# Kernel optimization log

Measured on AMD Instinct MI355X. Metric: run time of the kernel, lower is better.

## Reference

```python
import jax, jax.numpy as jnp
import numpy as np


def _sqdist(X1, X2):
    # squared euclidean distance matrix, matches torch.cdist(...,p=2)**2
    d2 = (jnp.sum(X1 * X1, -1)[:, None] + jnp.sum(X2 * X2, -1)[None, :]
          - 2.0 * (X1 @ X2.T))
    return jnp.maximum(d2, 0.0)


def setup_inputs() -> dict:
    key = jax.random.key(0)
    k1, k2, k3, k4, k5, k6 = jax.random.split(key, 6)
    n, m, d, C = 1024, 2048, 4, 64
    X_train = jax.random.normal(k1, (n, d), dtype=jnp.float32)
    y_train = jax.random.normal(k2, (n,), dtype=jnp.float32)
    X_test = jax.random.normal(k3, (m, d), dtype=jnp.float32)
    # positive params within the priors' supports
    lengthscale = jax.random.uniform(k4, (C,), minval=0.1, maxval=3.0, dtype=jnp.float32)
    variance = jax.random.uniform(k5, (C,), minval=0.1, maxval=3.0, dtype=jnp.float32)
    noise = jax.random.uniform(k6, (C,), minval=0.01, maxval=0.5, dtype=jnp.float32)
    return {"X_train": X_train, "y_train": y_train, "X_test": X_test,
            "lengthscale": lengthscale, "variance": variance, "noise": noise}


def reference(X_train, y_train, X_test, lengthscale, variance, noise):
    n = X_train.shape[0]
    ls2 = (lengthscale ** 2)[:, None, None]          # [C,1,1]
    var = variance[:, None, None]                     # [C,1,1]
    d2_tr = _sqdist(X_train, X_train)                 # [n,n]
    d2_te = _sqdist(X_test, X_train)                  # [m,n]
    K_train = var * jnp.exp(-0.5 * d2_tr[None] / ls2)   # [C,n,n]
    K_test = var * jnp.exp(-0.5 * d2_te[None] / ls2)    # [C,m,n]
    K_noisy = K_train + noise[:, None, None] * jnp.eye(n, dtype=K_train.dtype)
    L = jnp.linalg.cholesky(K_noisy)                  # batched [C,n,n]

    def per_chain(Lc, Ktc):
        solve = jax.scipy.linalg.solve_triangular
        z = solve(Lc, y_train, lower=True)            # [n]
        alpha = solve(Lc, z, lower=True, trans=1)     # [n]
        pred_mean = Ktc @ alpha                       # [m]
        v = solve(Lc, Ktc.T, lower=True)              # [n,m]
        pred_var = jnp.sum(v * v, axis=0)             # [m]
        return pred_mean, pred_var

    means, vars_ = jax.vmap(per_chain)(L, K_test)     # [C,m] each
    return means.mean(axis=0), vars_.mean(axis=0)
```

## Files before the change

kernel.cpp:

```cpp
#include <hip/hip_runtime.h>
#include <hip/hip_fp16.h>
#include <math.h>

#define N 1024
#define M 2048
#define C 64
#define NB 128
#define TB 8
#define NBLK 36
#define PL ((size_t)NBLK*NB*NB)

typedef __attribute__((ext_vector_type(8))) short bf16x8;
typedef __attribute__((ext_vector_type(8))) _Float16 f16x8;
typedef __attribute__((ext_vector_type(4))) float f32x4;

__device__ __forceinline__ size_t pblk(int ib, int jt){
    return ((size_t)((ib*(ib+1))/2 + jt))*((size_t)NB*NB);
}

#define TT(r,c) T[(r)][(((c)+(r)) & 127)]


__device__ __forceinline__ float sqdist4(const float4 a, const float4 b){
    float dx=a.x-b.x, dy=a.y-b.y, dz=a.z-b.z, dw=a.w-b.w;
    return dx*dx+dy*dy+dz*dz+dw*dw;
}

__device__ __forceinline__ void split4(float x0, float x1, float x2, float x3,
                                       uint2& hi, uint2& lo){
    unsigned b0=__float_as_uint(x0), b1=__float_as_uint(x1),
             b2=__float_as_uint(x2), b3=__float_as_uint(x3);
    unsigned h0=b0&0xFFFF0000u, h1=b1&0xFFFF0000u, h2=b2&0xFFFF0000u, h3=b3&0xFFFF0000u;
    hi.x = (h0>>16)|h1;  hi.y = (h2>>16)|h3;
    float l0=x0-__uint_as_float(h0), l1=x1-__uint_as_float(h1),
          l2=x2-__uint_as_float(h2), l3=x3-__uint_as_float(h3);
    lo.x = (__float_as_uint(l0)>>16) | (__float_as_uint(l1)&0xFFFF0000u);
    lo.y = (__float_as_uint(l2)>>16) | (__float_as_uint(l3)&0xFFFF0000u);
}

__device__ void chol_invert_lds(float T[NB][NB], int tid){
    for (int j = 0; j < NB; j++){
        float d = TT(j,j);
        float inv = 1.0f / sqrtf(d);
        for (int i = j+1+tid; i < NB; i += 256) TT(i,j) *= inv;
        if (tid == 0) TT(j,j) = d * inv;
        __syncthreads();
        int i = j+1 + (tid >> 1);
        if (i < NB){
            float lij = TT(i,j);
            for (int k = j+1+(tid&1); k <= i; k += 2)
                TT(i,k) -= lij * TT(k,j);
        }
        __syncthreads();
    }
    for (int i = 0; i < NB; i++){
        float inv_ii = 1.0f / TT(i,i);
        int j = tid & 127, hi = tid >> 7;
        float S = 0.0f;
        if (j < i){
            for (int k = i-1-hi; k >= j; k -= 2)
                S += TT(i,k) * TT(k,j);
        }
        if (hi && j < i) TT(j,i) = S;
        __syncthreads();
        if (!hi){
            if (j < i)      TT(i,j) = -inv_ii * (S + TT(j,i));
            else if (j == i) TT(i,i) = inv_ii;
        }
        __syncthreads();
    }
}


struct FragLds { __half Ah[4096], Al[4096], Bh[4096], Bl[4096]; };

__device__ __forceinline__ void stage_f16(__half* __restrict__ Hh, __half* __restrict__ Hl,
                                          const float* __restrict__ S, int ld,
                                          int k0, bool contig, int tid){
    #pragma unroll
    for (int h = 0; h < 2; h++){
        int u = tid + h*256;
        int fr = u & 15, kg = (u>>4)&3, rt = (u>>6)&3, hf = u>>8;
        int rc = hf*64 + rt*16 + fr;
        int kk = k0 + kg*8;
        float x[8];
        if (contig){
            float4 v0 = *(const float4*)&S[(size_t)rc*ld + kk];
            float4 v1 = *(const float4*)&S[(size_t)rc*ld + kk + 4];
            x[0]=v0.x;x[1]=v0.y;x[2]=v0.z;x[3]=v0.w;
            x[4]=v1.x;x[5]=v1.y;x[6]=v1.z;x[7]=v1.w;
        } else {
            #pragma unroll
            for (int e=0;e<8;e++) x[e] = S[(size_t)(kk+e)*ld + rc];
        }
        union { __half h[8]; uint4 u4; } Hi, Lo;
        #pragma unroll
        for (int e=0;e<8;e++){
            __half hv = __float2half_rn(x[e]);
            Hi.h[e] = hv;
            Lo.h[e] = __float2half_rn(x[e] - __half2float(hv));
        }
        *(uint4*)&Hh[(size_t)u*8] = Hi.u4;
        *(uint4*)&Hl[(size_t)u*8] = Lo.u4;
    }
}

__device__ __forceinline__ void mfma_slab_f16(const __half* Ah, const __half* Al,
                                              const __half* Bh, const __half* Bl,
                                              int wrow, int wcol, int lane,
                                              f32x4 acc[4][4]){
    f16x8 ah[4], al[4];
    #pragma unroll
    for (int rt=0;rt<4;rt++){
        ah[rt] = *(const f16x8*)&Ah[((size_t)((wrow*4+rt)*64 + lane))*8];
        al[rt] = *(const f16x8*)&Al[((size_t)((wrow*4+rt)*64 + lane))*8];
    }
    #pragma unroll
    for (int ct=0;ct<4;ct++){
        f16x8 bh = *(const f16x8*)&Bh[((size_t)((wcol*4+ct)*64 + lane))*8];
        f16x8 bl = *(const f16x8*)&Bl[((size_t)((wcol*4+ct)*64 + lane))*8];
        #pragma unroll
        for (int rt=0;rt<4;rt++){
            f32x4 a = acc[rt][ct];
            a = __builtin_amdgcn_mfma_f32_16x16x32_f16(ah[rt], bh, a, 0,0,0);
            a = __builtin_amdgcn_mfma_f32_16x16x32_f16(ah[rt], bl, a, 0,0,0);
            a = __builtin_amdgcn_mfma_f32_16x16x32_f16(al[rt], bh, a, 0,0,0);
            acc[rt][ct] = a;
        }
    }
}

__device__ void gemm_f16_unit(const float* __restrict__ A, int lda,
                              const float* __restrict__ B, int ldb, bool bContig,
                              FragLds& F, f32x4 acc[4][4], int tid){
    int lane = tid & 63, w = tid >> 6, wrow = w>>1, wcol = w&1;
    for (int k0 = 0; k0 < NB; k0 += 32){
        __syncthreads();
        stage_f16(F.Ah, F.Al, A, lda, k0, true, tid);
        stage_f16(F.Bh, F.Bl, B, ldb, k0, bContig, tid);
        __syncthreads();
        mfma_slab_f16(F.Ah, F.Al, F.Bh, F.Bl, wrow, wcol, lane, acc);
    }
}

__device__ __forceinline__ void store_f16acc(float* __restrict__ Cp, int ldc,
                                             const f32x4 acc[4][4], float sgn, int tid){
    int lane = tid&63, w = tid>>6, wrow = w>>1, wcol = w&1;
    int fr = lane&15, kg = lane>>4;
    #pragma unroll
    for (int rt=0;rt<4;rt++)
      #pragma unroll
      for (int ct=0;ct<4;ct++)
        #pragma unroll
        for (int r=0;r<4;r++){
            int row = wrow*64 + rt*16 + kg*4 + r;
            int col = wcol*64 + ct*16 + fr;
            Cp[(size_t)row*ldc + col] = sgn*acc[rt][ct][r];
        }
}

#define ZERO_ACC(acc) { _Pragma("unroll") for (int zi=0;zi<4;zi++) _Pragma("unroll") for (int zj=0;zj<4;zj++) acc[zi][zj] = (f32x4)0.0f; }


__global__ void k_init_acc(float* __restrict__ acc){
    int i = blockIdx.x*blockDim.x + threadIdx.x;
    if (i < 2*M) acc[i] = 0.0f;
}

__global__ void k_build_d2te(const float* __restrict__ Xtr, const float* __restrict__ Xte,
                             float* __restrict__ d2){
    int j = blockIdx.x;
    float4 xj = ((const float4*)Xte)[j];
    for (int i = threadIdx.x; i < N; i += blockDim.x){
        float4 xi = ((const float4*)Xtr)[i];
        d2[(size_t)j*N + i] = sqdist4(xi,xj);
    }
}

__global__ __launch_bounds__(256) void k_build_K(const float* __restrict__ Xtr,
                          const float* __restrict__ ls,
                          const float* __restrict__ var, const float* __restrict__ noise,
                          float* __restrict__ Lbuf){
    __shared__ float4 xr[NB], xc[NB];
    int c = blockIdx.y, flat = blockIdx.x;
    int ib = 0; while ((ib+1)*(ib+2)/2 <= flat) ib++;
    int jt = flat - ib*(ib+1)/2;
    int tid = threadIdx.x;
    if (tid < NB) xr[tid] = ((const float4*)Xtr)[ib*NB + tid];
    else          xc[tid-NB] = ((const float4*)Xtr)[jt*NB + (tid-NB)];
    __syncthreads();
    float il2 = 1.0f/(ls[c]*ls[c]);
    float vc = var[c], nc = noise[c];
    float* blk = Lbuf + c*PL + pblk(ib,jt);
    for (int idx = tid; idx < NB*NB; idx += 256){
        int r = idx >> 7, col = idx & 127;
        float d2v = sqdist4(xr[r], xc[col]);
        float v = vc*__expf(-0.5f*d2v*il2);
        if (ib==jt && r==col) v += nc;
        blk[idx] = v;
    }
}

__global__ __launch_bounds__(256) void k_diagF(float* __restrict__ Lbuf){
    __shared__ float T[NB][NB];
    int c = blockIdx.x, tid = threadIdx.x;
    float* A = Lbuf + c*PL + pblk(0,0);
    for (int idx = tid; idx < NB*NB; idx += 256){
        int r = idx >> 7, col = idx & 127;
        TT(r,col) = A[idx];
    }
    __syncthreads();
    chol_invert_lds(T, tid);
    for (int idx = tid; idx < NB*NB; idx += 256){
        int r = idx >> 7, col = idx & 127;
        A[idx] = (col <= r) ? TT(r,col) : 0.0f;
    }
}

__global__ __launch_bounds__(256) void k_panel(float* __restrict__ Lbuf, int kb){
    __shared__ FragLds F;
    int c = blockIdx.x;
    int ib = kb + 1 + blockIdx.y;
    int tid = threadIdx.x;
    float* base = Lbuf + c*PL;
    float* Ablk = base + pblk(ib,kb);
    const float* Dv = base + pblk(kb,kb);
    f32x4 acc[4][4]; ZERO_ACC(acc);
    gemm_f16_unit(Ablk, NB, Dv, NB, true, F, acc, tid);
    store_f16acc(Ablk, NB, acc, 1.0f, tid);
}

union SmU2 { FragLds f; float T[NB][NB]; };
__global__ __launch_bounds__(256) void k_syrk(float* __restrict__ Lbuf, int kb){
    __shared__ SmU2 sm;
    int c = blockIdx.x;
    int flat = blockIdx.y;
    int di = 0; while ((di+1)*(di+2)/2 <= flat) di++;
    int dj = flat - di*(di+1)/2;
    int i = kb+1+di, j = kb+1+dj;
    int tid = threadIdx.x;
    float* base = Lbuf + c*PL;
    float* Cblk = base + pblk(i,j);
    const float* Ablk = base + pblk(i,kb);
    const float* Bblk = base + pblk(j,kb);
    f32x4 acc[4][4]; ZERO_ACC(acc);
    gemm_f16_unit(Ablk, NB, Bblk, NB, true, sm.f, acc, tid);
    int lane = tid&63, w = tid>>6, wrow = w>>1, wcol = w&1;
    int fr = lane&15, kg = lane>>4;
    if (flat != 0){
        #pragma unroll
        for (int rt=0;rt<4;rt++)
          #pragma unroll
          for (int ct=0;ct<4;ct++)
            #pragma unroll
            for (int r=0;r<4;r++){
                int row = wrow*64 + rt*16 + kg*4 + r;
                int col = wcol*64 + ct*16 + fr;
                Cblk[(size_t)row*NB + col] -= acc[rt][ct][r];
            }
    } else {
        __syncthreads();
        float (*T)[NB] = sm.T;
        #pragma unroll
        for (int rt=0;rt<4;rt++)
          #pragma unroll
          for (int ct=0;ct<4;ct++)
            #pragma unroll
            for (int r=0;r<4;r++){
                int row = wrow*64 + rt*16 + kg*4 + r;
                int col = wcol*64 + ct*16 + fr;
                TT(row,col) = Cblk[(size_t)row*NB + col] - acc[rt][ct][r];
            }
        __syncthreads();
        chol_invert_lds(T, tid);
        for (int idx = tid; idx < NB*NB; idx += 256){
            int r = idx >> 7, col = idx & 127;
            Cblk[idx] = (col <= r) ? TT(r,col) : 0.0f;
        }
    }
}

__global__ __launch_bounds__(256) void k_gemmA(float* __restrict__ Trow,
                                               const float* __restrict__ Lbuf, int ib){
    __shared__ FragLds F;
    int c = blockIdx.x, ct = blockIdx.y;
    int tid = threadIdx.x;
    const float* base = Lbuf + c*PL;
    const float* Dv = base + pblk(ib,ib);
    const float* Bsrc = base + pblk(ib,ct);
    f32x4 acc[4][4]; ZERO_ACC(acc);
    gemm_f16_unit(Dv, NB, Bsrc, NB, false, F, acc, tid);
    store_f16acc(Trow + (size_t)c*NB*N + ct*NB, N, acc, 1.0f, tid);
}

__global__ __launch_bounds__(256) void k_gemmB(float* __restrict__ Lbuf,
                                               const float* __restrict__ Trow, int ib){
    __shared__ FragLds F;
    int c = blockIdx.x, jt = blockIdx.y;
    int tid = threadIdx.x;
    const float* G = Trow + (size_t)c*NB*N;
    float* base = Lbuf + c*PL;
    f32x4 acc[4][4]; ZERO_ACC(acc);
    for (int kt = jt; kt < ib; kt++)
        gemm_f16_unit(G + kt*NB, N, base + pblk(kt,jt), NB, false, F, acc, tid);
    store_f16acc(base + pblk(ib,jt), NB, acc, -1.0f, tid);
}

__global__ void k_zvec(const float* __restrict__ Lbuf, const float* __restrict__ y,
                       float* __restrict__ z){
    int c = blockIdx.x;
    int p = blockIdx.y * 4 + (threadIdx.x >> 6);
    int lane = threadIdx.x & 63;
    int pb = p >> 7, pl = p & 127;
    const float* base = Lbuf + c*PL;
    float s = 0.0f;
    for (int kt = 0; kt <= pb; kt++){
        const float* row = base + pblk(pb,kt) + (size_t)pl*NB;
        int lim = (kt==pb) ? pl : NB-1;
        for (int i = lane; i <= lim; i += 64) s += row[i]*y[kt*NB + i];
    }
    for (int off = 32; off; off >>= 1) s += __shfl_down(s, off);
    if (lane == 0) z[c*N + p] = s;
}

__global__ __launch_bounds__(256) void k_wsplit(float* __restrict__ Lbuf){
    int c = blockIdx.y, flat = blockIdx.x;
    int tid = threadIdx.x;
    float* blk = Lbuf + c*PL + (size_t)flat*NB*NB;
    float4 v[16];
    #pragma unroll
    for (int h = 0; h < 8; h++){
        int g = tid + h*256;
        int u = g & 511, slab = g >> 9;
        int fr = u&15, kg = (u>>4)&3, rt = (u>>6)&3, hf = u>>8;
        int row = hf*64 + rt*16 + fr;
        int k = slab*32 + kg*8;
        v[2*h]   = *(const float4*)&blk[(size_t)row*NB + k];
        v[2*h+1] = *(const float4*)&blk[(size_t)row*NB + k + 4];
    }
    __syncthreads();
    unsigned short* out = (unsigned short*)blk;
    #pragma unroll
    for (int h = 0; h < 8; h++){
        int g = tid + h*256;
        int u = g & 511, slab = g >> 9;
        uint2 h0, l0, h1, l1;
        split4(v[2*h].x, v[2*h].y, v[2*h].z, v[2*h].w, h0, l0);
        split4(v[2*h+1].x, v[2*h+1].y, v[2*h+1].z, v[2*h+1].w, h1, l1);
        *(uint4*)&out[((size_t)(slab*2+0)*512 + u)*8] = make_uint4(h0.x,h0.y,h1.x,h1.y);
        *(uint4*)&out[((size_t)(slab*2+1)*512 + u)*8] = make_uint4(l0.x,l0.y,l1.x,l1.y);
    }
}

__global__ __launch_bounds__(256) void k_bigg(const float* __restrict__ Lbuf,
                                              const float* __restrict__ d2,
                                              const float* __restrict__ zbuf,
                                              const float* __restrict__ ls,
                                              const float* __restrict__ var,
                                              float* __restrict__ acc_out){
    __shared__ unsigned short Ah[4096], Al[4096], Bh[4096], Bl[4096];
    int jt = blockIdx.x, pt = blockIdx.y, c = blockIdx.z;
    int tid = threadIdx.x;
    int lane = tid & 63, w = tid >> 6;
    int wrow = w >> 1, wcol = w & 1;
    float il2 = 1.0f/(ls[c]*ls[c]);
    float vc = var[c];
    float ec = -0.5f*il2;
    const float* Arow = d2 + (size_t)(jt*NB)*N;
    const float* Wbase = Lbuf + c*PL;
    int klen = (pt+1)*NB;
    f32x4 acc[4][4]; ZERO_ACC(acc);

    int fr = lane & 15, kg = lane >> 4;
    int q = tid & 7, rs = tid >> 3;
    int kgq = q >> 1, e4 = (q & 1) * 4;

    for (int k0 = 0; k0 < klen; k0 += 32){
        const unsigned short* Wimg = (const unsigned short*)(Wbase + pblk(pt, k0 >> 7));
        int slab = (k0 & 127) >> 5;
        const unsigned short* hi_img = Wimg + (size_t)(slab*2+0)*4096;
        const unsigned short* lo_img = Wimg + (size_t)(slab*2+1)*4096;
        __syncthreads();
        #pragma unroll
        for (int p = 0; p < 4; p++){
            int row = rs + 32*p;
            float4 dv = *(const float4*)&Arow[(size_t)row*N + k0 + q*4];
            float x0 = vc*__expf(ec*dv.x), x1 = vc*__expf(ec*dv.y);
            float x2 = vc*__expf(ec*dv.z), x3 = vc*__expf(ec*dv.w);
            uint2 hi, lo; split4(x0,x1,x2,x3, hi, lo);
            int u = (row&15) + kgq*16 + ((row>>4)&3)*64 + (row>>6)*256;
            *(uint2*)&Ah[(size_t)u*8 + e4] = hi;
            *(uint2*)&Al[(size_t)u*8 + e4] = lo;
        }
        #pragma unroll
        for (int h2 = 0; h2 < 2; h2++){
            int u = tid + h2*256;
            *(uint4*)&Bh[(size_t)u*8] = *(const uint4*)&hi_img[(size_t)u*8];
            *(uint4*)&Bl[(size_t)u*8] = *(const uint4*)&lo_img[(size_t)u*8];
        }
        __syncthreads();
        bf16x8 ah[4], al[4];
        #pragma unroll
        for (int rt=0;rt<4;rt++){
            ah[rt] = *(const bf16x8*)&Ah[((size_t)((wrow*4+rt)*64 + lane))*8];
            al[rt] = *(const bf16x8*)&Al[((size_t)((wrow*4+rt)*64 + lane))*8];
        }
        #pragma unroll
        for (int ct=0;ct<4;ct++){
            bf16x8 bh = *(const bf16x8*)&Bh[((size_t)((wcol*4+ct)*64 + lane))*8];
            bf16x8 bl = *(const bf16x8*)&Bl[((size_t)((wcol*4+ct)*64 + lane))*8];
            #pragma unroll
            for (int rt=0;rt<4;rt++){
                f32x4 a = acc[rt][ct];
                a = __builtin_amdgcn_mfma_f32_16x16x32_bf16(ah[rt], bh, a, 0,0,0);
                a = __builtin_amdgcn_mfma_f32_16x16x32_bf16(ah[rt], bl, a, 0,0,0);
                a = __builtin_amdgcn_mfma_f32_16x16x32_bf16(al[rt], bh, a, 0,0,0);
                acc[rt][ct] = a;
            }
        }
    }
    float zv[4];
    #pragma unroll
    for (int ct=0;ct<4;ct++) zv[ct] = zbuf[c*N + pt*NB + wcol*64 + ct*16 + fr];
    #pragma unroll
    for (int rt=0;rt<4;rt++){
        #pragma unroll
        for (int r=0;r<4;r++){
            float m = 0.0f, v = 0.0f;
            #pragma unroll
            for (int ct=0;ct<4;ct++){
                float x = acc[rt][ct][r];
                v += x*x; m += x*zv[ct];
            }
            m += __shfl_xor(m, 1);  v += __shfl_xor(v, 1);
            m += __shfl_xor(m, 2);  v += __shfl_xor(v, 2);
            m += __shfl_xor(m, 4);  v += __shfl_xor(v, 4);
            m += __shfl_xor(m, 8);  v += __shfl_xor(v, 8);
            if (fr == 0){
                int j = jt*NB + wrow*64 + rt*16 + kg*4 + r;
                atomicAdd(&acc_out[j], m);
                atomicAdd(&acc_out[M + j], v);
            }
        }
    }
}

__global__ void k_final(const float* __restrict__ acc, float* __restrict__ out){
    int i = blockIdx.x*blockDim.x + threadIdx.x;
    if (i < 2*M) out[i] = acc[i] * (1.0f/64.0f);
}


extern "C" void kernel_launch(void* const* d_in, const int* in_sizes, int n_in,
                              void* d_out, int out_size, void* d_ws, size_t ws_size,
                              hipStream_t stream) {
    const float* Xtr = (const float*)d_in[0];
    const float* ytr = (const float*)d_in[1];
    const float* Xte = (const float*)d_in[2];
    const float* ls  = (const float*)d_in[3];
    const float* var = (const float*)d_in[4];
    const float* noi = (const float*)d_in[5];
    float* out = (float*)d_out;

    float* ws = (float*)d_ws;
    const size_t shared_fl  = (size_t)N*M + 2*M;
    const size_t perchain   = PL + (size_t)NB*N + (size_t)N;
    size_t avail = ws_size / sizeof(float);
    if (avail < shared_fl + perchain) return;
    int Gmax = (int)((avail - shared_fl) / perchain);
    if (Gmax > C) Gmax = C;
    int nbatch = (C + Gmax - 1) / Gmax;
    int G = (C + nbatch - 1) / nbatch;

    float* d2te = ws;
    float* acc  = d2te + (size_t)N*M;
    float* Lbuf = acc  + 2*M;
    float* Trow = Lbuf + (size_t)G*PL;
    float* zbuf = Trow + (size_t)G*NB*N;

    k_init_acc<<<dim3((2*M+255)/256), dim3(256), 0, stream>>>(acc);
    k_build_d2te<<<dim3(M), dim3(256), 0, stream>>>(Xtr, Xte, d2te);

    for (int c0 = 0; c0 < C; c0 += G){
        int g = C - c0 < G ? C - c0 : G;

        k_build_K<<<dim3(NBLK, g), dim3(256), 0, stream>>>(Xtr, ls+c0, var+c0, noi+c0, Lbuf);
        k_diagF<<<dim3(g), dim3(256), 0, stream>>>(Lbuf);

        for (int kb = 0; kb < TB-1; kb++){
            int rem = TB-1-kb;
            k_panel<<<dim3(g, rem), dim3(256), 0, stream>>>(Lbuf, kb);
            k_syrk<<<dim3(g, rem*(rem+1)/2), dim3(256), 0, stream>>>(Lbuf, kb);
        }
        for (int ib = 1; ib < TB; ib++){
            k_gemmA<<<dim3(g, ib), dim3(256), 0, stream>>>(Trow, Lbuf, ib);
            k_gemmB<<<dim3(g, ib), dim3(256), 0, stream>>>(Lbuf, Trow, ib);
        }
        k_zvec<<<dim3(g, N/4), dim3(256), 0, stream>>>(Lbuf, ytr, zbuf);
        k_wsplit<<<dim3(NBLK, g), dim3(256), 0, stream>>>(Lbuf);
        k_bigg<<<dim3(M/NB, TB, g), dim3(256), 0, stream>>>(Lbuf, d2te, zbuf, ls+c0, var+c0, acc);
    }
    k_final<<<dim3((2*M+255)/256), dim3(256), 0, stream>>>(acc, out);
}
```

Measured before the change: 5.532 ms.

## Fuse diagonal factorization into K build, hoist variance scaling, swap bigg grid order

The first diagonal block's Cholesky/inversion now runs inside k_build_K, in the block that builds it, so the separate k_diagF launch is dropped. The variance multiply is taken out of the per-element exp in k_bigg and applied once to the reduced sums (vc for the mean, vc² for the variance). The k_bigg grid swaps its x and y dimensions so consecutive blocks share the same test-row tile. Chain offsets are also widened to size_t. The trade-off is that one build_K block now carries a serial factorization while the others finish early.

```diff
diff --git a/kernel.cpp b/kernel.cpp
--- a/kernel.cpp
+++ b/kernel.cpp
@@ -73,6 +73,8 @@
 
 
 struct FragLds { __half Ah[4096], Al[4096], Bh[4096], Bl[4096]; };
+struct SmX { float4 xr[NB]; float4 xc[NB]; };
+union SmU { FragLds f; float T[NB][NB]; SmX x; };
 
 __device__ __forceinline__ void stage_f16(__half* __restrict__ Hh, __half* __restrict__ Hl,
                                           const float* __restrict__ S, int ld,
@@ -177,43 +179,47 @@
     }
 }
 
+__global__ void k_final(const float* __restrict__ acc, float* __restrict__ out){
+    int i = blockIdx.x*blockDim.x + threadIdx.x;
+    if (i < 2*M) out[i] = acc[i] * (1.0f/64.0f);
+}
+
 __global__ __launch_bounds__(256) void k_build_K(const float* __restrict__ Xtr,
                           const float* __restrict__ ls,
                           const float* __restrict__ var, const float* __restrict__ noise,
                           float* __restrict__ Lbuf){
-    __shared__ float4 xr[NB], xc[NB];
+    __shared__ SmU sm;
     int c = blockIdx.y, flat = blockIdx.x;
     int ib = 0; while ((ib+1)*(ib+2)/2 <= flat) ib++;
     int jt = flat - ib*(ib+1)/2;
     int tid = threadIdx.x;
-    if (tid < NB) xr[tid] = ((const float4*)Xtr)[ib*NB + tid];
-    else          xc[tid-NB] = ((const float4*)Xtr)[jt*NB + (tid-NB)];
+    if (tid < NB) sm.x.xr[tid] = ((const float4*)Xtr)[ib*NB + tid];
+    else          sm.x.xc[tid-NB] = ((const float4*)Xtr)[jt*NB + (tid-NB)];
     __syncthreads();
     float il2 = 1.0f/(ls[c]*ls[c]);
     float vc = var[c], nc = noise[c];
     float* blk = Lbuf + c*PL + pblk(ib,jt);
     for (int idx = tid; idx < NB*NB; idx += 256){
         int r = idx >> 7, col = idx & 127;
-        float d2v = sqdist4(xr[r], xc[col]);
+        float d2v = sqdist4(sm.x.xr[r], sm.x.xc[col]);
         float v = vc*__expf(-0.5f*d2v*il2);
         if (ib==jt && r==col) v += nc;
         blk[idx] = v;
     }
-}
-
-__global__ __launch_bounds__(256) void k_diagF(float* __restrict__ Lbuf){
-    __shared__ float T[NB][NB];
-    int c = blockIdx.x, tid = threadIdx.x;
-    float* A = Lbuf + c*PL + pblk(0,0);
-    for (int idx = tid; idx < NB*NB; idx += 256){
-        int r = idx >> 7, col = idx & 127;
-        TT(r,col) = A[idx];
-    }
-    __syncthreads();
-    chol_invert_lds(T, tid);
-    for (int idx = tid; idx < NB*NB; idx += 256){
-        int r = idx >> 7, col = idx & 127;
-        A[idx] = (col <= r) ? TT(r,col) : 0.0f;
+    if (flat == 0){
+        __threadfence_block();
+        __syncthreads();
+        float (*T)[NB] = sm.T;
+        for (int idx = tid; idx < NB*NB; idx += 256){
+            int r = idx >> 7, col = idx & 127;
+            TT(r,col) = blk[idx];
+        }
+        __syncthreads();
+        chol_invert_lds(T, tid);
+        for (int idx = tid; idx < NB*NB; idx += 256){
+            int r = idx >> 7, col = idx & 127;
+            blk[idx] = (col <= r) ? TT(r,col) : 0.0f;
+        }
     }
 }
 
@@ -222,7 +228,7 @@
     int c = blockIdx.x;
     int ib = kb + 1 + blockIdx.y;
     int tid = threadIdx.x;
-    float* base = Lbuf + c*PL;
+    float* base = Lbuf + (size_t)c*PL;
     float* Ablk = base + pblk(ib,kb);
     const float* Dv = base + pblk(kb,kb);
     f32x4 acc[4][4]; ZERO_ACC(acc);
@@ -230,16 +236,15 @@
     store_f16acc(Ablk, NB, acc, 1.0f, tid);
 }
 
-union SmU2 { FragLds f; float T[NB][NB]; };
 __global__ __launch_bounds__(256) void k_syrk(float* __restrict__ Lbuf, int kb){
-    __shared__ SmU2 sm;
+    __shared__ SmU sm;
     int c = blockIdx.x;
     int flat = blockIdx.y;
     int di = 0; while ((di+1)*(di+2)/2 <= flat) di++;
     int dj = flat - di*(di+1)/2;
     int i = kb+1+di, j = kb+1+dj;
     int tid = threadIdx.x;
-    float* base = Lbuf + c*PL;
+    float* base = Lbuf + (size_t)c*PL;
     float* Cblk = base + pblk(i,j);
     const float* Ablk = base + pblk(i,kb);
     const float* Bblk = base + pblk(j,kb);
@@ -285,7 +290,7 @@
     __shared__ FragLds F;
     int c = blockIdx.x, ct = blockIdx.y;
     int tid = threadIdx.x;
-    const float* base = Lbuf + c*PL;
+    const float* base = Lbuf + (size_t)c*PL;
     const float* Dv = base + pblk(ib,ib);
     const float* Bsrc = base + pblk(ib,ct);
     f32x4 acc[4][4]; ZERO_ACC(acc);
@@ -299,7 +304,7 @@
     int c = blockIdx.x, jt = blockIdx.y;
     int tid = threadIdx.x;
     const float* G = Trow + (size_t)c*NB*N;
-    float* base = Lbuf + c*PL;
+    float* base = Lbuf + (size_t)c*PL;
     f32x4 acc[4][4]; ZERO_ACC(acc);
     for (int kt = jt; kt < ib; kt++)
         gemm_f16_unit(G + kt*NB, N, base + pblk(kt,jt), NB, false, F, acc, tid);
@@ -312,7 +317,7 @@
     int p = blockIdx.y * 4 + (threadIdx.x >> 6);
     int lane = threadIdx.x & 63;
     int pb = p >> 7, pl = p & 127;
-    const float* base = Lbuf + c*PL;
+    const float* base = Lbuf + (size_t)c*PL;
     float s = 0.0f;
     for (int kt = 0; kt <= pb; kt++){
         const float* row = base + pblk(pb,kt) + (size_t)pl*NB;
@@ -359,7 +364,7 @@
                                               const float* __restrict__ var,
                                               float* __restrict__ acc_out){
     __shared__ unsigned short Ah[4096], Al[4096], Bh[4096], Bl[4096];
-    int jt = blockIdx.x, pt = blockIdx.y, c = blockIdx.z;
+    int pt = blockIdx.x, jt = blockIdx.y, c = blockIdx.z;
     int tid = threadIdx.x;
     int lane = tid & 63, w = tid >> 6;
     int wrow = w >> 1, wcol = w & 1;
@@ -367,7 +372,7 @@
     float vc = var[c];
     float ec = -0.5f*il2;
     const float* Arow = d2 + (size_t)(jt*NB)*N;
-    const float* Wbase = Lbuf + c*PL;
+    const float* Wbase = Lbuf + (size_t)c*PL;
     int klen = (pt+1)*NB;
     f32x4 acc[4][4]; ZERO_ACC(acc);
 
@@ -385,8 +390,8 @@
         for (int p = 0; p < 4; p++){
             int row = rs + 32*p;
             float4 dv = *(const float4*)&Arow[(size_t)row*N + k0 + q*4];
-            float x0 = vc*__expf(ec*dv.x), x1 = vc*__expf(ec*dv.y);
-            float x2 = vc*__expf(ec*dv.z), x3 = vc*__expf(ec*dv.w);
+            float x0 = __expf(ec*dv.x), x1 = __expf(ec*dv.y);
+            float x2 = __expf(ec*dv.z), x3 = __expf(ec*dv.w);
             uint2 hi, lo; split4(x0,x1,x2,x3, hi, lo);
             int u = (row&15) + kgq*16 + ((row>>4)&3)*64 + (row>>6)*256;
             *(uint2*)&Ah[(size_t)u*8 + e4] = hi;
@@ -419,6 +424,7 @@
             }
         }
     }
+    float vc2 = vc*vc;
     float zv[4];
     #pragma unroll
     for (int ct=0;ct<4;ct++) zv[ct] = zbuf[c*N + pt*NB + wcol*64 + ct*16 + fr];
@@ -438,16 +444,11 @@
             m += __shfl_xor(m, 8);  v += __shfl_xor(v, 8);
             if (fr == 0){
                 int j = jt*NB + wrow*64 + rt*16 + kg*4 + r;
-                atomicAdd(&acc_out[j], m);
-                atomicAdd(&acc_out[M + j], v);
+                atomicAdd(&acc_out[j], vc*m);
+                atomicAdd(&acc_out[M + j], vc2*v);
             }
         }
     }
-}
-
-__global__ void k_final(const float* __restrict__ acc, float* __restrict__ out){
-    int i = blockIdx.x*blockDim.x + threadIdx.x;
-    if (i < 2*M) out[i] = acc[i] * (1.0f/64.0f);
 }
 
 
@@ -485,7 +486,6 @@
         int g = C - c0 < G ? C - c0 : G;
 
         k_build_K<<<dim3(NBLK, g), dim3(256), 0, stream>>>(Xtr, ls+c0, var+c0, noi+c0, Lbuf);
-        k_diagF<<<dim3(g), dim3(256), 0, stream>>>(Lbuf);
 
         for (int kb = 0; kb < TB-1; kb++){
             int rem = TB-1-kb;
@@ -498,7 +498,7 @@
         }
         k_zvec<<<dim3(g, N/4), dim3(256), 0, stream>>>(Lbuf, ytr, zbuf);
         k_wsplit<<<dim3(NBLK, g), dim3(256), 0, stream>>>(Lbuf);
-        k_bigg<<<dim3(M/NB, TB, g), dim3(256), 0, stream>>>(Lbuf, d2te, zbuf, ls+c0, var+c0, acc);
+        k_bigg<<<dim3(TB, M/NB, g), dim3(256), 0, stream>>>(Lbuf, d2te, zbuf, ls+c0, var+c0, acc);
     }
     k_final<<<dim3((2*M+255)/256), dim3(256), 0, stream>>>(acc, out);
 }
```

Result: slower. 5.799 ms (+4.8%).
